# Kernel tuning notes

Measured on AMD Instinct MI355X. Metric: run time of the kernel, lower is better.

Reference implementation:

```python
import jax, jax.numpy as jnp
import numpy as np

TGT, BSZ, E, H, HD, P = 256, 64, 1024, 16, 64, 16
TAU = 3.0  # gumbel temperature
SCALE = 1.0 / np.sqrt(HD)


def setup_inputs() -> dict:
    rng = jax.random.key(0)
    ks = jax.random.split(rng, 14)
    n = lambda i, s: jax.random.normal(ks[i], s, dtype=jnp.float32)
    u = jax.random.uniform(ks[7], (BSZ, 2), dtype=jnp.float32, minval=1e-6, maxval=1.0 - 1e-6)
    return {
        'idx': 0,
        'query': n(0, (TGT, BSZ, E)),
        'key': n(1, (TGT, BSZ, E)),
        'value': n(2, (TGT, BSZ, E)),
        'prefix': n(3, (BSZ, 2, P, E)) * 0.5,  # gathered prefix_pool[prompt_ids]
        'batch_weight': jax.random.uniform(ks[4], (BSZ,), dtype=jnp.float32),
        'ori_image_features': n(5, (BSZ, 512)),
        'gumbel_noise': -jnp.log(-jnp.log(u)),  # standard gumbel(0,1) noise
        'in_proj_w': n(8, (3 * E, E)) * 0.02,
        'in_proj_b': jnp.zeros((3 * E,), jnp.float32),
        'out_w': n(9, (E, E)) * 0.02,
        'out_b': jnp.zeros((E,), jnp.float32),
        'gumbel_w': n(10, (2, 512)) * 0.05,
        'gumbel_b': jnp.zeros((2,), jnp.float32),
    }


def _sdpa(q, k, v):
    # q:[b,h,t,d] k,v:[b,h,s,d]
    s = jnp.einsum('bhtd,bhsd->bhts', q, k) * SCALE
    a = jax.nn.softmax(s, axis=-1)
    return jnp.einsum('bhts,bhsd->bhtd', a, v)


def reference(idx, query, key, value, prefix, batch_weight, ori_image_features,
              gumbel_noise, in_proj_w, in_proj_b, out_w, out_b, gumbel_w, gumbel_b):
    tgt, bsz, e = query.shape
    src = key.shape[0]
    # packed in-projection (w chunked into q/k/v blocks)
    w_q, w_k, w_v = jnp.split(in_proj_w, 3, axis=0)
    b_q, b_k, b_v = jnp.split(in_proj_b, 3, axis=0)
    q = query @ w_q.T + b_q            # [t,b,E]
    k = key @ w_k.T + b_k              # [s,b,E]
    v = value @ w_v.T + b_v
    # -> [b,h,t,d]
    q = q.reshape(tgt, bsz, H, HD).transpose(1, 2, 0, 3)
    k = k.reshape(src, bsz, H, HD).transpose(1, 2, 0, 3)
    v = v.reshape(src, bsz, H, HD).transpose(1, 2, 0, 3)
    # prefix k/v: [b,P,E] -> [b,h,P,d] (no in-projection, used raw as in source)
    pk = prefix[:, 0].reshape(bsz, P, H, HD).transpose(0, 2, 1, 3)
    pv = prefix[:, 1].reshape(bsz, P, H, HD).transpose(0, 2, 1, 3)

    attn = _sdpa(q, k, v)                      # [b,h,t,d]
    attn_flat = attn.transpose(2, 0, 1, 3).reshape(tgt * bsz, e)  # (t,b) row order

    attn_pre = _sdpa(q, pk, pv) * batch_weight[:, None, None, None]
    attn_pre_flat = attn_pre.transpose(2, 0, 1, 3).reshape(tgt * bsz, e)

    # gumbel-softmax gate (soft), one 2-way gate per sample
    logits = ori_image_features @ gumbel_w.T + gumbel_b           # [b,2]
    gumbel = jax.nn.softmax((logits + gumbel_noise) / TAU, axis=-1)
    gate = jnp.repeat(gumbel, tgt, axis=0)                        # [b*t,2] (b,t) order, as in source
    combined = attn_flat * gate[:, :1] + (attn_flat + attn_pre_flat) * gate[:, 1:2]

    out = combined @ out_w.T + out_b
    return out.reshape(tgt, bsz, e)
```

## Files before the change

### kernel.cpp

```cpp
#include <hip/hip_runtime.h>

typedef __attribute__((ext_vector_type(8))) short bf16x8;
typedef __attribute__((ext_vector_type(4))) float f32x4;
typedef __attribute__((ext_vector_type(8))) unsigned short ushort8;
typedef __attribute__((ext_vector_type(4))) unsigned short ushort4v;
typedef __attribute__((ext_vector_type(4))) float float4v;
typedef __attribute__((ext_vector_type(2))) unsigned int uint2v;

#define TGT 256
#define BSZ 64
#define EMB 1024
#define NH 16
#define HD 64
#define PP 16

__device__ __forceinline__ float b2f(unsigned short u) {
  return __builtin_bit_cast(float, ((unsigned int)u) << 16);
}
__device__ __forceinline__ unsigned short f2b(float f) {
  unsigned int u = __builtin_bit_cast(unsigned int, f);
  u += 0x7fffu + ((u >> 16) & 1u);
  return (unsigned short)(u >> 16);
}
__device__ __forceinline__ unsigned int pack2(float lo, float hi) {
  return (unsigned int)f2b(lo) | ((unsigned int)f2b(hi) << 16);
}
__device__ __forceinline__ f32x4 mfma16(bf16x8 a, bf16x8 b, f32x4 c) {
  return __builtin_amdgcn_mfma_f32_16x16x32_bf16(a, b, c, 0, 0, 0);
}
__device__ __forceinline__ void gl_lds16(const unsigned short* g, unsigned short* l) {
  __builtin_amdgcn_global_load_lds(
      (const __attribute__((address_space(1))) unsigned int*)g,
      (__attribute__((address_space(3))) unsigned int*)l, 16, 0, 0);
}

__global__ __launch_bounds__(64) void gate_kernel(
    const float* __restrict__ feat, const float* __restrict__ gw,
    const float* __restrict__ gb, const float* __restrict__ noise,
    float* __restrict__ g1) {
  const int b = blockIdx.x, lane = threadIdx.x;
  float a0 = 0.f, a1 = 0.f;
  for (int i = lane; i < 512; i += 64) {
    float f = feat[b * 512 + i];
    a0 += f * gw[i];
    a1 += f * gw[512 + i];
  }
#pragma unroll
  for (int off = 32; off >= 1; off >>= 1) {
    a0 += __shfl_xor(a0, off);
    a1 += __shfl_xor(a1, off);
  }
  if (lane == 0) {
    float l0 = (a0 + gb[0] + noise[b * 2 + 0]) * (1.0f / 3.0f);
    float l1 = (a1 + gb[1] + noise[b * 2 + 1]) * (1.0f / 3.0f);
    float mm = fmaxf(l0, l1);
    float e0 = __expf(l0 - mm), e1 = __expf(l1 - mm);
    g1[b] = e1 / (e0 + e1);
  }
}

__global__ __launch_bounds__(256) void cast_bf16_kernel(
    const float* __restrict__ in, unsigned short* __restrict__ out, int n8) {
  int i = blockIdx.x * blockDim.x + threadIdx.x;
  const int stride = gridDim.x * blockDim.x;
  for (; i < n8; i += stride) {
    const float4v* p = (const float4v*)(in + (size_t)i * 8);
    float4v v0 = p[0], v1 = p[1];
    ushort8 o = {f2b(v0[0]), f2b(v0[1]), f2b(v0[2]), f2b(v0[3]),
                 f2b(v1[0]), f2b(v1[1]), f2b(v1[2]), f2b(v1[3])};
    *(ushort8*)(out + (size_t)i * 8) = o;
  }
}

#define AOFF(s) (A_BLOCKED ? (((s) >> 1) * 16384 + ((s)&1) * 32) : (s)*32)
#define STAGE_A(s)                                       \
  {                                                      \
    const unsigned short* _ap = a0p + AOFF(s);           \
    unsigned short* d = &As[(s) & 3][wl];                \
    gl_lds16(_ap, d);                                    \
    gl_lds16(_ap + aD, d + 4096);                        \
  }
#define STAGE_B(s)                                       \
  {                                                      \
    int k0s = (s) * 32;                                  \
    unsigned short* d = &Bs[(s) & 3][wl];                \
    gl_lds16(b0p + k0s, d);                              \
    gl_lds16(b1p + k0s, d + 4096);                       \
  }
#define GEMM_STEP(s, DO_STAGE)                                        \
  {                                                                   \
    const unsigned short* Ab = &As[(s) & 3][0];                       \
    const unsigned short* Bb = &Bs[(s) & 3][0];                       \
    bf16x8 af[8], bfr[4];                                             \
    _Pragma("unroll") for (int mi = 0; mi < 8; ++mi)                  \
        af[mi] = *(const bf16x8*)&Ab[aoff + mi * 512];                \
    _Pragma("unroll") for (int ni = 0; ni < 2; ++ni)                  \
        bfr[ni] = *(const bf16x8*)&Bb[boff + ni * 512];               \
    if (DO_STAGE) STAGE_A((s) + 3);                                   \
    __builtin_amdgcn_s_barrier();                                     \
    __builtin_amdgcn_s_setprio(1);                                    \
    _Pragma("unroll") for (int mi = 0; mi < 8; ++mi) {                \
      acc[mi][0] = mfma16(af[mi], bfr[0], acc[mi][0]);                \
      acc[mi][1] = mfma16(af[mi], bfr[1], acc[mi][1]);                \
    }                                                                 \
    __builtin_amdgcn_s_setprio(0);                                    \
    __builtin_amdgcn_s_barrier();                                     \
    _Pragma("unroll") for (int ni = 2; ni < 4; ++ni)                  \
        bfr[ni] = *(const bf16x8*)&Bb[boff + ni * 512];               \
    if (DO_STAGE) STAGE_B((s) + 3);                                   \
    __builtin_amdgcn_s_barrier();                                     \
    __builtin_amdgcn_s_setprio(1);                                    \
    _Pragma("unroll") for (int mi = 0; mi < 8; ++mi) {                \
      acc[mi][2] = mfma16(af[mi], bfr[2], acc[mi][2]);                \
      acc[mi][3] = mfma16(af[mi], bfr[3], acc[mi][3]);                \
    }                                                                 \
    __builtin_amdgcn_s_setprio(0);                                    \
  }
#define STEP_WAIT(cntstr)                                \
  asm volatile("s_waitcnt " cntstr ::: "memory");        \
  __builtin_amdgcn_sched_barrier(0);                     \
  __builtin_amdgcn_s_barrier();

template <int OUT_F32, int QSCALE, int A_BLOCKED>
__global__ __launch_bounds__(512, 2) void gemm256_kernel(
    const unsigned short* __restrict__ A, const unsigned short* __restrict__ W,
    const float* __restrict__ bias, void* __restrict__ Cv) {
  constexpr int K = 1024, N = 1024;
  __shared__ __attribute__((aligned(16))) unsigned short As[4][8192];
  __shared__ __attribute__((aligned(16))) unsigned short Bs[4][8192];
  const int tid = threadIdx.x;
  const int wv = tid >> 6, lane = tid & 63;
  const int l15 = lane & 15, kg = lane >> 4;
  const int bid = blockIdx.x;
  const int cpx = gridDim.x >> 3;
  const int wg = (bid & 7) * cpx + (bid >> 3);
  const int m0 = (wg >> 2) * 256, n0 = (wg & 3) * 256;
  const int wmL = (wv >> 2) * 128, wnL = (wv & 3) * 64;

  const int sr = wv * 16 + (lane >> 2);
  const int sc = ((lane & 3) * 8) ^ (((sr >> 1) & 3) << 3);
  const int srg = m0 + sr;
  const unsigned short* a0p;
  if constexpr (A_BLOCKED)
    a0p = A + (size_t)(srg & 63) * 262144 + (srg >> 6) * 64 + sc;
  else
    a0p = A + (size_t)srg * K + sc;
  const int aD = A_BLOCKED ? 128 : 128 * K;
  const unsigned short* b0p = W + (size_t)(n0 + sr) * K + sc;
  const unsigned short* b1p = b0p + (size_t)128 * K;
  const int wl = wv * 512;

  const int x = ((l15 >> 1) & 3) << 3;
  const int aoff = (wmL + l15) * 32 + ((kg * 8) ^ x);
  const int boff = (wnL + l15) * 32 + ((kg * 8) ^ x);

  f32x4 acc[8][4];
#pragma unroll
  for (int i = 0; i < 8; ++i)
#pragma unroll
    for (int j = 0; j < 4; ++j) acc[i][j] = (f32x4){0.f, 0.f, 0.f, 0.f};

  STAGE_A(0); STAGE_B(0); STAGE_A(1); STAGE_B(1); STAGE_A(2); STAGE_B(2);
  STEP_WAIT("vmcnt(8)")

  for (int s = 0; s < 29; ++s) {
    GEMM_STEP(s, 1);
    STEP_WAIT("vmcnt(8)")
  }
  GEMM_STEP(29, 0);
  STEP_WAIT("vmcnt(4)")
  GEMM_STEP(30, 0);
  STEP_WAIT("vmcnt(0)")
  GEMM_STEP(31, 0);

#pragma unroll
  for (int mi = 0; mi < 8; ++mi) {
#pragma unroll
    for (int ni = 0; ni < 4; ++ni) {
      int col = n0 + wnL + ni * 16 + l15;
      float bcol = bias[col];
#pragma unroll
      for (int r = 0; r < 4; ++r) {
        int row = m0 + wmL + mi * 16 + kg * 4 + r;
        float v = acc[mi][ni][r] + bcol;
        if constexpr (QSCALE) v *= 0.125f;
        if constexpr (OUT_F32) {
          ((float*)Cv)[(size_t)row * N + col] = v;
        } else {
          int t = row >> 6, bb = row & 63, hh = col >> 6, dd = col & 63;
          ((unsigned short*)Cv)[(size_t)((bb * 16 + hh) * 256 + t) * 64 + dd] = f2b(v);
        }
      }
    }
  }
}

__global__ __launch_bounds__(512) void attn_kernel(
    const unsigned short* __restrict__ qb, const unsigned short* __restrict__ kb,
    const unsigned short* __restrict__ vb, const float* __restrict__ prefix,
    const float* __restrict__ bw, const float* __restrict__ g1,
    unsigned short* __restrict__ comb) {
  const int b = blockIdx.x, h = blockIdx.y;
  __shared__ __attribute__((aligned(16))) unsigned short Kl[256][64];
  __shared__ __attribute__((aligned(16))) unsigned short Vt[64 * 256];
  __shared__ __attribute__((aligned(16))) unsigned short PKl[16][64];
  __shared__ __attribute__((aligned(16))) unsigned short PVt[64][32];
  __shared__ __attribute__((aligned(16))) unsigned short Plds[8][16][40];
  unsigned short* Cb = &Kl[0][0];
  const int tid = threadIdx.x;
  const int wv = tid >> 6, lane = tid & 63;
  const size_t slab = (size_t)(b * NH + h) * 16384;

#pragma unroll
  for (int it = 0; it < 4; ++it) {
    int cid = tid + it * 512;
    int j = cid >> 3, c = cid & 7;
    gl_lds16(kb + slab + (size_t)j * 64 + ((c ^ (j & 7)) << 3),
             &Kl[0][0] + (size_t)(it * 512 + wv * 64) * 8);
    ushort8 vv = *(const ushort8*)(vb + slab + (size_t)j * 64 + (c << 3));
#pragma unroll
    for (int i = 0; i < 8; ++i) {
      int gran = (j >> 3) ^ i ^ c;
      Vt[(c * 8 + i) * 256 + gran * 8 + (j & 7)] = vv[i];
    }
  }
  if (tid < 256) {
    int arr = tid >> 7, cid = tid & 127;
    int sp = cid >> 3, c = cid & 7;
    const float* src = prefix + ((size_t)(b * 2 + arr) * PP + sp) * EMB + h * HD + c * 8;
    float4v v0 = *(const float4v*)src;
    float4v v1 = *(const float4v*)(src + 4);
    if (arr == 0) {
      ushort8 o = {f2b(v0[0]), f2b(v0[1]), f2b(v0[2]), f2b(v0[3]),
                   f2b(v1[0]), f2b(v1[1]), f2b(v1[2]), f2b(v1[3])};
      *(ushort8*)&PKl[sp][((c ^ (sp & 7)) << 3)] = o;
    } else {
#pragma unroll
      for (int i = 0; i < 8; ++i)
        PVt[c * 8 + i][sp] = f2b(i < 4 ? v0[i] : v1[i - 4]);
    }
  } else if (tid < 384) {
    int cid = tid - 256;
    *(ushort8*)&PVt[cid >> 1][16 + (cid & 1) * 8] = (ushort8){0, 0, 0, 0, 0, 0, 0, 0};
  }
  __syncthreads();

  const int l15 = lane & 15, g = lane >> 4;
  const int swl = l15 & 7;
  const float bwb = bw[b];
  unsigned short(&Pw)[16][40] = Plds[wv];

  const int t0 = wv * 32 + l15;
  const size_t qbase = slab + (size_t)t0 * 64;
  bf16x8 qf[2][2];
  qf[0][0] = *(const bf16x8*)(qb + qbase + g * 8);
  qf[0][1] = *(const bf16x8*)(qb + qbase + 32 + g * 8);
  qf[1][0] = *(const bf16x8*)(qb + qbase + 1024 + g * 8);
  qf[1][1] = *(const bf16x8*)(qb + qbase + 1024 + 32 + g * 8);

  f32x4 O[2][4];
#pragma unroll
  for (int st = 0; st < 2; ++st)
#pragma unroll
    for (int dt = 0; dt < 4; ++dt) O[st][dt] = (f32x4){0.f, 0.f, 0.f, 0.f};
  float m[2] = {-3.0e38f, -3.0e38f}, l[2] = {0.f, 0.f};

#pragma unroll
  for (int ch = 0; ch < 8; ++ch) {
    const int rA = ch * 32 + l15, rB = rA + 16;
    bf16x8 ka0 = *(const bf16x8*)&Kl[rA][((g ^ swl) << 3)];
    bf16x8 ka1 = *(const bf16x8*)&Kl[rA][(((4 + g) ^ swl) << 3)];
    bf16x8 kb0 = *(const bf16x8*)&Kl[rB][((g ^ swl) << 3)];
    bf16x8 kb1 = *(const bf16x8*)&Kl[rB][(((4 + g) ^ swl) << 3)];
    f32x4 s[2][2];
#pragma unroll
    for (int st = 0; st < 2; ++st) {
      s[st][0] = (f32x4){0.f, 0.f, 0.f, 0.f};
      s[st][1] = (f32x4){0.f, 0.f, 0.f, 0.f};
      s[st][0] = mfma16(ka0, qf[st][0], s[st][0]);
      s[st][0] = mfma16(ka1, qf[st][1], s[st][0]);
      s[st][1] = mfma16(kb0, qf[st][0], s[st][1]);
      s[st][1] = mfma16(kb1, qf[st][1], s[st][1]);
    }
    bf16x8 pf[2];
#pragma unroll
    for (int st = 0; st < 2; ++st) {
      f32x4 sa = s[st][0], sb = s[st][1];
      float mx = fmaxf(fmaxf(fmaxf(sa[0], sa[1]), fmaxf(sa[2], sa[3])),
                       fmaxf(fmaxf(sb[0], sb[1]), fmaxf(sb[2], sb[3])));
      mx = fmaxf(mx, __shfl_xor(mx, 16));
      mx = fmaxf(mx, __shfl_xor(mx, 32));
      if (__ballot(mx > m[st] + 8.0f) != 0ull) {
        float mn = fmaxf(m[st], mx);
        float f = __expf(m[st] - mn);
        m[st] = mn;
        l[st] *= f;
#pragma unroll
        for (int dt = 0; dt < 4; ++dt)
#pragma unroll
          for (int r = 0; r < 4; ++r) O[st][dt][r] *= f;
      }
      float pA[4], pB[4];
#pragma unroll
      for (int r = 0; r < 4; ++r) {
        pA[r] = __expf(sa[r] - m[st]);
        pB[r] = __expf(sb[r] - m[st]);
      }
      uint2v wa = {pack2(pA[0], pA[1]), pack2(pA[2], pA[3])};
      uint2v wb2 = {pack2(pB[0], pB[1]), pack2(pB[2], pB[3])};
      *(uint2v*)&Pw[l15][g * 4] = wa;
      *(uint2v*)&Pw[l15][16 + g * 4] = wb2;
      float sloc = b2f((unsigned short)(wa[0] & 0xffff)) + b2f((unsigned short)(wa[0] >> 16)) +
                   b2f((unsigned short)(wa[1] & 0xffff)) + b2f((unsigned short)(wa[1] >> 16)) +
                   b2f((unsigned short)(wb2[0] & 0xffff)) + b2f((unsigned short)(wb2[0] >> 16)) +
                   b2f((unsigned short)(wb2[1] & 0xffff)) + b2f((unsigned short)(wb2[1] >> 16));
      l[st] += sloc;
      pf[st] = *(const bf16x8*)&Pw[l15][g * 8];
    }
#pragma unroll
    for (int dt = 0; dt < 4; ++dt) {
      const int drow = dt * 16 + l15;
      const int gran = (ch * 4 + g) ^ (drow & 7) ^ (drow >> 3);
      bf16x8 vf = *(const bf16x8*)&Vt[drow * 256 + gran * 8];
      O[0][dt] = mfma16(vf, pf[0], O[0][dt]);
      O[1][dt] = mfma16(vf, pf[1], O[1][dt]);
    }
  }

#pragma unroll
  for (int st = 0; st < 2; ++st) {
    float lf = l[st];
    lf += __shfl_xor(lf, 16);
    lf += __shfl_xor(lf, 32);
    float inv = 1.0f / lf;
#pragma unroll
    for (int dt = 0; dt < 4; ++dt)
#pragma unroll
      for (int r = 0; r < 4; ++r) O[st][dt][r] *= inv;
  }

  {
    bf16x8 pk0 = *(const bf16x8*)&PKl[l15][((g ^ swl) << 3)];
    bf16x8 pk1 = *(const bf16x8*)&PKl[l15][(((4 + g) ^ swl) << 3)];
    bf16x8 ppf[2];
#pragma unroll
    for (int st = 0; st < 2; ++st) {
      f32x4 sp4 = (f32x4){0.f, 0.f, 0.f, 0.f};
      sp4 = mfma16(pk0, qf[st][0], sp4);
      sp4 = mfma16(pk1, qf[st][1], sp4);
      float pm = fmaxf(fmaxf(sp4[0], sp4[1]), fmaxf(sp4[2], sp4[3]));
      pm = fmaxf(pm, __shfl_xor(pm, 16));
      pm = fmaxf(pm, __shfl_xor(pm, 32));
      float pe[4], pl = 0.f;
#pragma unroll
      for (int r = 0; r < 4; ++r) {
        pe[r] = __expf(sp4[r] - pm);
        pl += pe[r];
      }
      pl += __shfl_xor(pl, 16);
      pl += __shfl_xor(pl, 32);
      float cpre = g1[(t0 + 16 * st) >> 2] * bwb / pl;
#pragma unroll
      for (int r = 0; r < 4; ++r) pe[r] *= cpre;
      *(uint2v*)&Pw[l15][g * 4] = (uint2v){pack2(pe[0], pe[1]), pack2(pe[2], pe[3])};
      *(uint2v*)&Pw[l15][16 + g * 4] = (uint2v){0u, 0u};
      ppf[st] = *(const bf16x8*)&Pw[l15][g * 8];
    }
#pragma unroll
    for (int dt = 0; dt < 4; ++dt) {
      bf16x8 pvf = *(const bf16x8*)&PVt[dt * 16 + l15][g * 8];
      O[0][dt] = mfma16(pvf, ppf[0], O[0][dt]);
      O[1][dt] = mfma16(pvf, ppf[1], O[1][dt]);
    }
  }

  __syncthreads();
#pragma unroll
  for (int st = 0; st < 2; ++st) {
    int t = wv * 32 + st * 16 + l15;
#pragma unroll
    for (int dt = 0; dt < 4; ++dt) {
#pragma unroll
      for (int u = 0; u < 2; ++u) {
        unsigned int pw = pack2(O[st][dt][2 * u], O[st][dt][2 * u + 1]);
        int d = dt * 16 + g * 4 + 2 * u;
        *(unsigned int*)&Cb[t * 64 + (((d >> 3) ^ (t & 7)) << 3) + (d & 7)] = pw;
      }
    }
  }
  __syncthreads();
#pragma unroll
  for (int it = 0; it < 4; ++it) {
    int cid = tid + it * 512;
    int j = cid >> 3, c = cid & 7;
    ushort8 row = *(const ushort8*)&Cb[j * 64 + ((c ^ (j & 7)) << 3)];
    *(ushort8*)(comb + slab + (size_t)j * 64 + (c << 3)) = row;
  }
}

extern "C" void kernel_launch(void* const* d_in, const int* in_sizes, int n_in,
                              void* d_out, int out_size, void* d_ws, size_t ws_size,
                              hipStream_t stream) {
  const float* query = (const float*)d_in[1];
  const float* key = (const float*)d_in[2];
  const float* value = (const float*)d_in[3];
  const float* prefix = (const float*)d_in[4];
  const float* bw = (const float*)d_in[5];
  const float* feat = (const float*)d_in[6];
  const float* noise = (const float*)d_in[7];
  const float* ipw = (const float*)d_in[8];
  const float* ipb = (const float*)d_in[9];
  const float* outw = (const float*)d_in[10];
  const float* outb = (const float*)d_in[11];
  const float* gw = (const float*)d_in[12];
  const float* gb = (const float*)d_in[13];
  float* out = (float*)d_out;

  char* ws = (char*)d_ws;
  const size_t MATB = (size_t)16384 * 1024;
  unsigned short* qb = (unsigned short*)ws;
  unsigned short* kb = qb + MATB;
  unsigned short* vb = kb + MATB;
  unsigned short* cb = vb + MATB;
  unsigned short* wip = cb + MATB;
  unsigned short* wo = wip + (size_t)3072 * 1024;
  float* g1 = (float*)(wo + (size_t)1024 * 1024);

  gate_kernel<<<64, 64, 0, stream>>>(feat, gw, gb, noise, g1);

  cast_bf16_kernel<<<1536, 256, 0, stream>>>(ipw, wip, 3072 * 1024 / 8);
  cast_bf16_kernel<<<512, 256, 0, stream>>>(outw, wo, 1024 * 1024 / 8);

  const int N8 = (int)(MATB / 8);
  cast_bf16_kernel<<<2048, 256, 0, stream>>>(query, cb, N8);
  gemm256_kernel<0, 1, 0><<<256, 512, 0, stream>>>(cb, wip, ipb, qb);
  cast_bf16_kernel<<<2048, 256, 0, stream>>>(key, cb, N8);
  gemm256_kernel<0, 0, 0><<<256, 512, 0, stream>>>(cb, wip + (size_t)1024 * 1024, ipb + 1024, kb);
  cast_bf16_kernel<<<2048, 256, 0, stream>>>(value, cb, N8);
  gemm256_kernel<0, 0, 0><<<256, 512, 0, stream>>>(cb, wip + (size_t)2048 * 1024, ipb + 2048, vb);

  attn_kernel<<<dim3(64, 16), 512, 0, stream>>>(qb, kb, vb, prefix, bw, g1, cb);

  gemm256_kernel<1, 0, 1><<<256, 512, 0, stream>>>(cb, wo, outb, out);
}
```

Before: 279.0 us.

## Fuse fp32-to-bf16 activation cast into in-projection GEMM A-tile loading

```diff
diff --git a/kernel.cpp b/kernel.cpp
--- a/kernel.cpp
+++ b/kernel.cpp
@@ -6,6 +6,7 @@
 typedef __attribute__((ext_vector_type(4))) unsigned short ushort4v;
 typedef __attribute__((ext_vector_type(4))) float float4v;
 typedef __attribute__((ext_vector_type(2))) unsigned int uint2v;
+typedef __attribute__((ext_vector_type(4))) unsigned int uint4v;
 
 #define TGT 256
 #define BSZ 64
@@ -72,13 +73,32 @@
   }
 }
 
+#define ASLOT(s) ((s) & (A_F32 ? 1 : 3))
 #define AOFF(s) (A_BLOCKED ? (((s) >> 1) * 16384 + ((s)&1) * 32) : (s)*32)
 #define STAGE_A(s)                                       \
   {                                                      \
-    const unsigned short* _ap = a0p + AOFF(s);           \
-    unsigned short* d = &As[(s) & 3][wl];                \
+    const unsigned short* _ap = abf + AOFF(s);           \
+    unsigned short* d = &As[ASLOT(s)][wl];               \
     gl_lds16(_ap, d);                                    \
     gl_lds16(_ap + aD, d + 4096);                        \
+  }
+#define ISSUE_A32(t)                                     \
+  {                                                      \
+    const float* _p = a32p + (size_t)(t) * 32;           \
+    ar[0] = *(const float4v*)_p;                         \
+    ar[1] = *(const float4v*)(_p + 4);                   \
+    ar[2] = *(const float4v*)(_p + 131072);              \
+    ar[3] = *(const float4v*)(_p + 131072 + 4);          \
+  }
+#define WRITE_A32(t)                                                    \
+  {                                                                     \
+    uint4v h0 = {pack2(ar[0][0], ar[0][1]), pack2(ar[0][2], ar[0][3]),  \
+                 pack2(ar[1][0], ar[1][1]), pack2(ar[1][2], ar[1][3])}; \
+    uint4v h1 = {pack2(ar[2][0], ar[2][1]), pack2(ar[2][2], ar[2][3]),  \
+                 pack2(ar[3][0], ar[3][1]), pack2(ar[3][2], ar[3][3])}; \
+    unsigned short* d = &As[(t) & 1][swA];                              \
+    *(uint4v*)d = h0;                                                   \
+    *(uint4v*)(d + 4096) = h1;                                          \
   }
 #define STAGE_B(s)                                       \
   {                                                      \
@@ -87,16 +107,20 @@
     gl_lds16(b0p + k0s, d);                              \
     gl_lds16(b1p + k0s, d + 4096);                       \
   }
-#define GEMM_STEP(s, DO_STAGE)                                        \
+#define GEMM_STEP(s, DO_ISSUEA, DO_STAGEB, DO_WRITE)                  \
   {                                                                   \
-    const unsigned short* Ab = &As[(s) & 3][0];                       \
+    const unsigned short* Ab = &As[ASLOT(s)][0];                      \
     const unsigned short* Bb = &Bs[(s) & 3][0];                       \
     bf16x8 af[8], bfr[4];                                             \
     _Pragma("unroll") for (int mi = 0; mi < 8; ++mi)                  \
         af[mi] = *(const bf16x8*)&Ab[aoff + mi * 512];                \
     _Pragma("unroll") for (int ni = 0; ni < 2; ++ni)                  \
         bfr[ni] = *(const bf16x8*)&Bb[boff + ni * 512];               \
-    if (DO_STAGE) STAGE_A((s) + 3);                                   \
+    if constexpr (A_F32) {                                            \
+      if (DO_ISSUEA) ISSUE_A32((s) + 1);                              \
+    } else {                                                          \
+      if (DO_ISSUEA) STAGE_A((s) + 3);                                \
+    }                                                                 \
     __builtin_amdgcn_s_barrier();                                     \
     __builtin_amdgcn_s_setprio(1);                                    \
     _Pragma("unroll") for (int mi = 0; mi < 8; ++mi) {                \
@@ -107,7 +131,7 @@
     __builtin_amdgcn_s_barrier();                                     \
     _Pragma("unroll") for (int ni = 2; ni < 4; ++ni)                  \
         bfr[ni] = *(const bf16x8*)&Bb[boff + ni * 512];               \
-    if (DO_STAGE) STAGE_B((s) + 3);                                   \
+    if (DO_STAGEB) STAGE_B((s) + 3);                                  \
     __builtin_amdgcn_s_barrier();                                     \
     __builtin_amdgcn_s_setprio(1);                                    \
     _Pragma("unroll") for (int mi = 0; mi < 8; ++mi) {                \
@@ -115,18 +139,21 @@
       acc[mi][3] = mfma16(af[mi], bfr[3], acc[mi][3]);                \
     }                                                                 \
     __builtin_amdgcn_s_setprio(0);                                    \
+    if constexpr (A_F32) {                                            \
+      if (DO_WRITE) WRITE_A32((s) + 1);                               \
+    }                                                                 \
   }
 #define STEP_WAIT(cntstr)                                \
   asm volatile("s_waitcnt " cntstr ::: "memory");        \
   __builtin_amdgcn_sched_barrier(0);                     \
   __builtin_amdgcn_s_barrier();
 
-template <int OUT_F32, int QSCALE, int A_BLOCKED>
+template <int OUT_F32, int QSCALE, int A_BLOCKED, int A_F32>
 __global__ __launch_bounds__(512, 2) void gemm256_kernel(
-    const unsigned short* __restrict__ A, const unsigned short* __restrict__ W,
+    const void* __restrict__ Av, const unsigned short* __restrict__ W,
     const float* __restrict__ bias, void* __restrict__ Cv) {
   constexpr int K = 1024, N = 1024;
-  __shared__ __attribute__((aligned(16))) unsigned short As[4][8192];
+  __shared__ __attribute__((aligned(16))) unsigned short As[(A_F32 ? 2 : 4)][8192];
   __shared__ __attribute__((aligned(16))) unsigned short Bs[4][8192];
   const int tid = threadIdx.x;
   const int wv = tid >> 6, lane = tid & 63;
@@ -140,12 +167,15 @@
   const int sr = wv * 16 + (lane >> 2);
   const int sc = ((lane & 3) * 8) ^ (((sr >> 1) & 3) << 3);
   const int srg = m0 + sr;
-  const unsigned short* a0p;
+  const unsigned short* abf;
   if constexpr (A_BLOCKED)
-    a0p = A + (size_t)(srg & 63) * 262144 + (srg >> 6) * 64 + sc;
+    abf = (const unsigned short*)Av + (size_t)(srg & 63) * 262144 + (srg >> 6) * 64 + sc;
   else
-    a0p = A + (size_t)srg * K + sc;
+    abf = (const unsigned short*)Av + (size_t)srg * K + sc;
   const int aD = A_BLOCKED ? 128 : 128 * K;
+  const float* a32p = (const float*)Av + (size_t)srg * K + (lane & 3) * 8;
+  const int swA = sr * 32 + (((lane & 3) ^ ((sr >> 1) & 3)) << 3);
+  float4v ar[4];
   const unsigned short* b0p = W + (size_t)(n0 + sr) * K + sc;
   const unsigned short* b1p = b0p + (size_t)128 * K;
   const int wl = wv * 512;
@@ -160,18 +190,28 @@
 #pragma unroll
     for (int j = 0; j < 4; ++j) acc[i][j] = (f32x4){0.f, 0.f, 0.f, 0.f};
 
-  STAGE_A(0); STAGE_B(0); STAGE_A(1); STAGE_B(1); STAGE_A(2); STAGE_B(2);
-  STEP_WAIT("vmcnt(8)")
-
-  for (int s = 0; s < 29; ++s) {
-    GEMM_STEP(s, 1);
+  if constexpr (A_F32) {
+    ISSUE_A32(0); STAGE_B(0); STAGE_B(1); STAGE_B(2);
+    WRITE_A32(0);
+    STEP_WAIT("vmcnt(4) lgkmcnt(0)")
+    for (int s = 0; s < 31; ++s) {
+      GEMM_STEP(s, 1, (s < 29), 1);
+      STEP_WAIT("vmcnt(2) lgkmcnt(0)")
+    }
+    GEMM_STEP(31, 0, 0, 0);
+  } else {
+    STAGE_A(0); STAGE_B(0); STAGE_A(1); STAGE_B(1); STAGE_A(2); STAGE_B(2);
     STEP_WAIT("vmcnt(8)")
-  }
-  GEMM_STEP(29, 0);
-  STEP_WAIT("vmcnt(4)")
-  GEMM_STEP(30, 0);
-  STEP_WAIT("vmcnt(0)")
-  GEMM_STEP(31, 0);
+    for (int s = 0; s < 29; ++s) {
+      GEMM_STEP(s, 1, 1, 0);
+      STEP_WAIT("vmcnt(8)")
+    }
+    GEMM_STEP(29, 0, 0, 0);
+    STEP_WAIT("vmcnt(4)")
+    GEMM_STEP(30, 0, 0, 0);
+    STEP_WAIT("vmcnt(0)")
+    GEMM_STEP(31, 0, 0, 0);
+  }
 
 #pragma unroll
   for (int mi = 0; mi < 8; ++mi) {
@@ -431,15 +471,11 @@
   cast_bf16_kernel<<<1536, 256, 0, stream>>>(ipw, wip, 3072 * 1024 / 8);
   cast_bf16_kernel<<<512, 256, 0, stream>>>(outw, wo, 1024 * 1024 / 8);
 
-  const int N8 = (int)(MATB / 8);
-  cast_bf16_kernel<<<2048, 256, 0, stream>>>(query, cb, N8);
-  gemm256_kernel<0, 1, 0><<<256, 512, 0, stream>>>(cb, wip, ipb, qb);
-  cast_bf16_kernel<<<2048, 256, 0, stream>>>(key, cb, N8);
-  gemm256_kernel<0, 0, 0><<<256, 512, 0, stream>>>(cb, wip + (size_t)1024 * 1024, ipb + 1024, kb);
-  cast_bf16_kernel<<<2048, 256, 0, stream>>>(value, cb, N8);
-  gemm256_kernel<0, 0, 0><<<256, 512, 0, stream>>>(cb, wip + (size_t)2048 * 1024, ipb + 2048, vb);
+  gemm256_kernel<0, 1, 0, 1><<<256, 512, 0, stream>>>(query, wip, ipb, qb);
+  gemm256_kernel<0, 0, 0, 1><<<256, 512, 0, stream>>>(key, wip + (size_t)1024 * 1024, ipb + 1024, kb);
+  gemm256_kernel<0, 0, 0, 1><<<256, 512, 0, stream>>>(value, wip + (size_t)2048 * 1024, ipb + 2048, vb);
 
   attn_kernel<<<dim3(64, 16), 512, 0, stream>>>(qb, kb, vb, prefix, bw, g1, cb);
 
-  gemm256_kernel<1, 0, 1><<<256, 512, 0, stream>>>(cb, wo, outb, out);
-}
+  gemm256_kernel<1, 0, 1, 0><<<256, 512, 0, stream>>>(cb, wo, outb, out);
+}
```

Measured after the change: 306.5 us. +9.8%, slower.

## Fuse fp32-to-bf16 activation cast into 128-row QKV projection GEMM

Applied to the files above, without the earlier changes.

```diff
diff --git a/kernel.cpp b/kernel.cpp
--- a/kernel.cpp
+++ b/kernel.cpp
@@ -6,6 +6,7 @@
 typedef __attribute__((ext_vector_type(4))) unsigned short ushort4v;
 typedef __attribute__((ext_vector_type(4))) float float4v;
 typedef __attribute__((ext_vector_type(2))) unsigned int uint2v;
+typedef __attribute__((ext_vector_type(4))) unsigned int uint4v;
 
 #define TGT 256
 #define BSZ 64
@@ -72,13 +73,136 @@
   }
 }
 
-#define AOFF(s) (A_BLOCKED ? (((s) >> 1) * 16384 + ((s)&1) * 32) : (s)*32)
+#define A128_ISSUE(t)                                    \
+  {                                                      \
+    const float* _p = a32p + (size_t)(t) * 32;           \
+    ar[(t) & 1][0] = *(const float4v*)_p;                \
+    ar[(t) & 1][1] = *(const float4v*)(_p + 4);          \
+  }
+#define A128_WRITE(t)                                                   \
+  {                                                                     \
+    float4v* v = ar[(t) & 1];                                           \
+    uint4v h = {pack2(v[0][0], v[0][1]), pack2(v[0][2], v[0][3]),       \
+                pack2(v[1][0], v[1][1]), pack2(v[1][2], v[1][3])};      \
+    *(uint4v*)&As[(t) & 1][swA] = h;                                    \
+  }
+#define B128_STAGE(s)                                    \
+  {                                                      \
+    int k0s = (s) * 32;                                  \
+    unsigned short* d = &Bs[(s) & 3][wl];                \
+    gl_lds16(b0p + k0s, d);                              \
+    gl_lds16(b1p + k0s, d + 4096);                       \
+  }
+#define G128_STEP(s, DO_IA, DO_SB, DO_W)                              \
+  {                                                                   \
+    const unsigned short* Ab = &As[(s) & 1][0];                       \
+    const unsigned short* Bb = &Bs[(s) & 3][0];                       \
+    bf16x8 af[4], bfr[4];                                             \
+    _Pragma("unroll") for (int mi = 0; mi < 4; ++mi)                  \
+        af[mi] = *(const bf16x8*)&Ab[aoff + mi * 512];                \
+    _Pragma("unroll") for (int ni = 0; ni < 2; ++ni)                  \
+        bfr[ni] = *(const bf16x8*)&Bb[boff + ni * 512];               \
+    if (DO_IA) A128_ISSUE((s) + 2);                                   \
+    __builtin_amdgcn_s_barrier();                                     \
+    __builtin_amdgcn_s_setprio(1);                                    \
+    _Pragma("unroll") for (int mi = 0; mi < 4; ++mi) {                \
+      acc[mi][0] = mfma16(af[mi], bfr[0], acc[mi][0]);                \
+      acc[mi][1] = mfma16(af[mi], bfr[1], acc[mi][1]);                \
+    }                                                                 \
+    __builtin_amdgcn_s_setprio(0);                                    \
+    __builtin_amdgcn_s_barrier();                                     \
+    _Pragma("unroll") for (int ni = 2; ni < 4; ++ni)                  \
+        bfr[ni] = *(const bf16x8*)&Bb[boff + ni * 512];               \
+    if (DO_SB) B128_STAGE((s) + 3);                                   \
+    __builtin_amdgcn_s_barrier();                                     \
+    __builtin_amdgcn_s_setprio(1);                                    \
+    _Pragma("unroll") for (int mi = 0; mi < 4; ++mi) {                \
+      acc[mi][2] = mfma16(af[mi], bfr[2], acc[mi][2]);                \
+      acc[mi][3] = mfma16(af[mi], bfr[3], acc[mi][3]);                \
+    }                                                                 \
+    __builtin_amdgcn_s_setprio(0);                                    \
+    if (DO_W) A128_WRITE((s) + 1);                                    \
+  }
+#define STEP_WAIT(cntstr)                                \
+  asm volatile("s_waitcnt " cntstr ::: "memory");        \
+  __builtin_amdgcn_sched_barrier(0);                     \
+  __builtin_amdgcn_s_barrier();
+
+template <int QSCALE>
+__global__ __launch_bounds__(512, 4) void gemm128f_kernel(
+    const float* __restrict__ A, const unsigned short* __restrict__ W,
+    const float* __restrict__ bias, unsigned short* __restrict__ Cv) {
+  constexpr int K = 1024, N = 1024;
+  __shared__ __attribute__((aligned(16))) unsigned short As[2][4096];
+  __shared__ __attribute__((aligned(16))) unsigned short Bs[4][8192];
+  const int tid = threadIdx.x;
+  const int wv = tid >> 6, lane = tid & 63;
+  const int l15 = lane & 15, kg = lane >> 4;
+  const int bid = blockIdx.x;
+  const int cpx = gridDim.x >> 3;
+  const int wg = (bid & 7) * cpx + (bid >> 3);
+  const int m0 = (wg >> 2) * 128, n0 = (wg & 3) * 256;
+  const int wmL = (wv >> 2) * 64, wnL = (wv & 3) * 64;
+
+  const int sr = wv * 16 + (lane >> 2);
+  const int sc = ((lane & 3) * 8) ^ (((sr >> 1) & 3) << 3);
+  const unsigned short* b0p = W + (size_t)(n0 + sr) * K + sc;
+  const unsigned short* b1p = b0p + (size_t)128 * K;
+  const int wl = wv * 512;
+
+  const int arr = tid >> 2;
+  const float* a32p = A + (size_t)(m0 + arr) * K + (tid & 3) * 8;
+  const int swA = arr * 32 + (((tid & 3) ^ ((arr >> 1) & 3)) << 3);
+  float4v ar[2][2];
+
+  const int x = ((l15 >> 1) & 3) << 3;
+  const int aoff = (wmL + l15) * 32 + ((kg * 8) ^ x);
+  const int boff = (wnL + l15) * 32 + ((kg * 8) ^ x);
+
+  f32x4 acc[4][4];
+#pragma unroll
+  for (int i = 0; i < 4; ++i)
+#pragma unroll
+    for (int j = 0; j < 4; ++j) acc[i][j] = (f32x4){0.f, 0.f, 0.f, 0.f};
+
+  A128_ISSUE(0); B128_STAGE(0); A128_ISSUE(1); B128_STAGE(1); B128_STAGE(2);
+  A128_WRITE(0);
+  STEP_WAIT("vmcnt(6) lgkmcnt(0)")
+
+#pragma unroll
+  for (int s = 0; s < 30; ++s) {
+    G128_STEP(s, (s < 30), (s < 29), 1);
+    STEP_WAIT("vmcnt(6) lgkmcnt(0)")
+  }
+  G128_STEP(30, 0, 0, 1);
+  STEP_WAIT("vmcnt(0) lgkmcnt(0)")
+  G128_STEP(31, 0, 0, 0);
+
+#pragma unroll
+  for (int mi = 0; mi < 4; ++mi) {
+#pragma unroll
+    for (int ni = 0; ni < 4; ++ni) {
+      int col = n0 + wnL + ni * 16 + l15;
+      float bcol = bias[col];
+#pragma unroll
+      for (int r = 0; r < 4; ++r) {
+        int row = m0 + wmL + mi * 16 + kg * 4 + r;
+        float v = acc[mi][ni][r] + bcol;
+        if constexpr (QSCALE) v *= 0.125f;
+        int t = row >> 6, bb = row & 63, hh = col >> 6, dd = col & 63;
+        Cv[(size_t)((bb * 16 + hh) * 256 + t) * 64 + dd] = f2b(v);
+      }
+    }
+  }
+}
+
+#define AOFF(s) (((s) >> 1) * 16384 + ((s)&1) * 32)
 #define STAGE_A(s)                                       \
   {                                                      \
-    const unsigned short* _ap = a0p + AOFF(s);           \
+    const unsigned short* _ap = abf + AOFF(s);           \
     unsigned short* d = &As[(s) & 3][wl];                \
     gl_lds16(_ap, d);                                    \
-    gl_lds16(_ap + aD, d + 4096);                        \
+    gl_lds16(_ap + 128, d + 4096);                       \
   }
 #define STAGE_B(s)                                       \
   {                                                      \
@@ -116,15 +240,10 @@
     }                                                                 \
     __builtin_amdgcn_s_setprio(0);                                    \
   }
-#define STEP_WAIT(cntstr)                                \
-  asm volatile("s_waitcnt " cntstr ::: "memory");        \
-  __builtin_amdgcn_sched_barrier(0);                     \
-  __builtin_amdgcn_s_barrier();
-
-template <int OUT_F32, int QSCALE, int A_BLOCKED>
+
 __global__ __launch_bounds__(512, 2) void gemm256_kernel(
     const unsigned short* __restrict__ A, const unsigned short* __restrict__ W,
-    const float* __restrict__ bias, void* __restrict__ Cv) {
+    const float* __restrict__ bias, float* __restrict__ Cv) {
   constexpr int K = 1024, N = 1024;
   __shared__ __attribute__((aligned(16))) unsigned short As[4][8192];
   __shared__ __attribute__((aligned(16))) unsigned short Bs[4][8192];
@@ -140,12 +259,8 @@
   const int sr = wv * 16 + (lane >> 2);
   const int sc = ((lane & 3) * 8) ^ (((sr >> 1) & 3) << 3);
   const int srg = m0 + sr;
-  const unsigned short* a0p;
-  if constexpr (A_BLOCKED)
-    a0p = A + (size_t)(srg & 63) * 262144 + (srg >> 6) * 64 + sc;
-  else
-    a0p = A + (size_t)srg * K + sc;
-  const int aD = A_BLOCKED ? 128 : 128 * K;
+  const unsigned short* abf =
+      A + (size_t)(srg & 63) * 262144 + (srg >> 6) * 64 + sc;
   const unsigned short* b0p = W + (size_t)(n0 + sr) * K + sc;
   const unsigned short* b1p = b0p + (size_t)128 * K;
   const int wl = wv * 512;
@@ -182,14 +297,7 @@
 #pragma unroll
       for (int r = 0; r < 4; ++r) {
         int row = m0 + wmL + mi * 16 + kg * 4 + r;
-        float v = acc[mi][ni][r] + bcol;
-        if constexpr (QSCALE) v *= 0.125f;
-        if constexpr (OUT_F32) {
-          ((float*)Cv)[(size_t)row * N + col] = v;
-        } else {
-          int t = row >> 6, bb = row & 63, hh = col >> 6, dd = col & 63;
-          ((unsigned short*)Cv)[(size_t)((bb * 16 + hh) * 256 + t) * 64 + dd] = f2b(v);
-        }
+        Cv[(size_t)row * N + col] = acc[mi][ni][r] + bcol;
       }
     }
   }
@@ -431,15 +539,11 @@
   cast_bf16_kernel<<<1536, 256, 0, stream>>>(ipw, wip, 3072 * 1024 / 8);
   cast_bf16_kernel<<<512, 256, 0, stream>>>(outw, wo, 1024 * 1024 / 8);
 
-  const int N8 = (int)(MATB / 8);
-  cast_bf16_kernel<<<2048, 256, 0, stream>>>(query, cb, N8);
-  gemm256_kernel<0, 1, 0><<<256, 512, 0, stream>>>(cb, wip, ipb, qb);
-  cast_bf16_kernel<<<2048, 256, 0, stream>>>(key, cb, N8);
-  gemm256_kernel<0, 0, 0><<<256, 512, 0, stream>>>(cb, wip + (size_t)1024 * 1024, ipb + 1024, kb);
-  cast_bf16_kernel<<<2048, 256, 0, stream>>>(value, cb, N8);
-  gemm256_kernel<0, 0, 0><<<256, 512, 0, stream>>>(cb, wip + (size_t)2048 * 1024, ipb + 2048, vb);
+  gemm128f_kernel<1><<<512, 512, 0, stream>>>(query, wip, ipb, qb);
+  gemm128f_kernel<0><<<512, 512, 0, stream>>>(key, wip + (size_t)1024 * 1024, ipb + 1024, kb);
+  gemm128f_kernel<0><<<512, 512, 0, stream>>>(value, wip + (size_t)2048 * 1024, ipb + 2048, vb);
 
   attn_kernel<<<dim3(64, 16), 512, 0, stream>>>(qb, kb, vb, prefix, bw, g1, cb);
 
-  gemm256_kernel<1, 0, 1><<<256, 512, 0, stream>>>(cb, wo, outb, out);
-}
+  gemm256_kernel<<<256, 512, 0, stream>>>(cb, wo, outb, out);
+}
```

Result: no change. 274.2 us (-1.7%).
